# Performance work log

Measured on AMD Instinct MI355X. Metric: run time of the kernel, lower is better.

The kernel has to match this reference:

```python
import jax, jax.numpy as jnp
import numpy as np

N = 262144
H = 256
R = 32


def setup_inputs() -> dict:
    key = jax.random.key(0)
    ks = jax.random.split(key, 16)
    s = 1.0 / np.sqrt(H)
    return {
        "x": jax.random.normal(ks[0], (N, 1), jnp.float32),
        "t": jax.random.uniform(ks[1], (N, 1), jnp.float32),
        "start_w": jax.random.normal(ks[2], (H, 2), jnp.float32) * 0.5,
        "start_b": jax.random.normal(ks[3], (H,), jnp.float32) * 0.1,
        "end_w": jax.random.normal(ks[4], (1, H), jnp.float32) * s,
        "end_b": jax.random.normal(ks[5], (1,), jnp.float32) * 0.1,
        "col_0": jax.random.normal(ks[6], (H, R), jnp.float32) * s,
        "col_1": jax.random.normal(ks[7], (H, R), jnp.float32) * s,
        "col_2": jax.random.normal(ks[8], (H, R), jnp.float32) * s,
        "row_0": jax.random.normal(ks[9], (H, R), jnp.float32) * s,
        "row_1": jax.random.normal(ks[10], (H, R), jnp.float32) * s,
        "row_2": jax.random.normal(ks[11], (H, R), jnp.float32) * s,
        "alpha_0": jax.random.normal(ks[12], (R,), jnp.float32),
        "alpha_1": jax.random.normal(ks[13], (R,), jnp.float32),
        "alpha_2": jax.random.normal(ks[14], (R,), jnp.float32),
    }


def reference(x, t, start_w, start_b, end_w, end_b,
              col_0, col_1, col_2, row_0, row_1, row_2,
              alpha_0, alpha_1, alpha_2):
    # inputs: [N,2] -> start Linear -> tanh
    inp = jnp.concatenate([x, t], axis=1)
    h = jnp.tanh(inp @ start_w.T + start_b)  # [N, H]
    # three low-rank blocks: h @ (col * diag(alpha)) @ row.T, then tanh.
    # col_basis @ diag(alpha) == col_basis * alpha[None, :] (column scaling)
    for col, row, alpha in ((col_0, row_0, alpha_0),
                            (col_1, row_1, alpha_1),
                            (col_2, row_2, alpha_2)):
        h = jnp.tanh((h @ (col * alpha)) @ row.T)  # [N,H]->[N,R]->[N,H]
    return h @ end_w.T + end_b  # [N, 1]
```

## Files before the change

### kernel.cpp

```cpp
#include <hip/hip_runtime.h>


typedef _Float16 half4_t __attribute__((ext_vector_type(4)));
typedef __fp16   fp16x2  __attribute__((ext_vector_type(2)));
typedef float    float4_t __attribute__((ext_vector_type(4)));

#define TANH_SCALE 2.885390081777927f
#define MFMA16 __builtin_amdgcn_mfma_f32_16x16x16f16
#define NFRAG (3 * 16 * 2 * 64)

namespace {

struct alignas(16) Smem {
  half4_t ctf[NFRAG];
  float w0[256], w1[256], bb[256];
  float ew[256];
};

__device__ __forceinline__ half4_t pack4(float4_t v) {
  union { fp16x2 f2[2]; half4_t h4; } u;
  u.f2[0] = __builtin_amdgcn_cvt_pkrtz(v.x, v.y);
  u.f2[1] = __builtin_amdgcn_cvt_pkrtz(v.z, v.w);
  return u.h4;
}

__device__ __forceinline__ float tanh_pre(float y) {
  const float e = __builtin_amdgcn_exp2f(y);
  return fmaf(-2.0f, __builtin_amdgcn_rcpf(e + 1.0f), 1.0f);
}

__device__ __forceinline__ half4_t tanh4(float4_t v) {
  float4_t r;
  r.x = tanh_pre(v.x); r.y = tanh_pre(v.y);
  r.z = tanh_pre(v.z); r.w = tanh_pre(v.w);
  return pack4(r);
}

__global__ __launch_bounds__(1024) void stage_rwf(
    const float* __restrict__ r0, const float* __restrict__ r1,
    const float* __restrict__ r2, half4_t* __restrict__ ws)
{
  const int e = blockIdx.x * 1024 + threadIdx.x;
  if (e >= NFRAG) return;
  const int lane_ = e & 63;
  const int sel   = (e >> 6) & 1;
  const int t_    = (e >> 7) & 15;
  const int k_    = e >> 11;
  const int m_ = lane_ & 15, q_ = lane_ >> 4;
  const float* rk = (k_ == 0) ? r0 : (k_ == 1) ? r1 : r2;
  const int j = 16 * t_ + m_;
  const int rr = sel * 16 + 4 * q_;
  half4_t v;
  v.x = (_Float16)(rk[j * 32 + rr + 0] * TANH_SCALE);
  v.y = (_Float16)(rk[j * 32 + rr + 1] * TANH_SCALE);
  v.z = (_Float16)(rk[j * 32 + rr + 2] * TANH_SCALE);
  v.w = (_Float16)(rk[j * 32 + rr + 3] * TANH_SCALE);
  ws[e] = v;
}

__global__ __launch_bounds__(1024)
__attribute__((amdgpu_waves_per_eu(8, 8)))
void pinn_fused(
    const float* __restrict__ xg, const float* __restrict__ tg,
    const float* __restrict__ sw, const float* __restrict__ sb,
    const float* __restrict__ ewp, const float* __restrict__ ebp,
    const float* __restrict__ c0, const float* __restrict__ c1,
    const float* __restrict__ c2, const float* __restrict__ a0,
    const float* __restrict__ a1, const float* __restrict__ a2,
    const half4_t* __restrict__ rwg, float* __restrict__ out, int n)
{
  __shared__ Smem sm;
  const int tid = threadIdx.x;

  for (int e = tid; e < NFRAG; e += 1024) {
    const int lane_ = e & 63;
    const int sel   = (e >> 6) & 1;
    const int t_    = (e >> 7) & 15;
    const int k_    = e >> 11;
    const int m_ = lane_ & 15, q_ = lane_ >> 4;
    const float* ck = (k_ == 0) ? c0 : (k_ == 1) ? c1 : c2;
    const float* ak = (k_ == 0) ? a0 : (k_ == 1) ? a1 : a2;
    const int r = sel * 16 + m_;
    const float av = ak[r];
    const int j0 = 16 * t_ + 4 * q_;
    half4_t v;
    v.x = (_Float16)(ck[(j0 + 0) * 32 + r] * av);
    v.y = (_Float16)(ck[(j0 + 1) * 32 + r] * av);
    v.z = (_Float16)(ck[(j0 + 2) * 32 + r] * av);
    v.w = (_Float16)(ck[(j0 + 3) * 32 + r] * av);
    sm.ctf[e] = v;
  }
  if (tid < 256) {
    sm.w0[tid] = sw[2 * tid] * TANH_SCALE;
    sm.w1[tid] = sw[2 * tid + 1] * TANH_SCALE;
    sm.bb[tid] = sb[tid] * TANH_SCALE;
    sm.ew[tid] = ewp[tid];
  }
  __syncthreads();

  const int wave = tid >> 6;
  const int lane = tid & 63;
  const int m = lane & 15;
  const int q = lane >> 4;
  const int wo = 4 * q;
  const float ebv = ebp[0];
  const int tiles = n >> 4;

  const float4_t z4 = {0.f, 0.f, 0.f, 0.f};

#pragma unroll 1
  for (int g = (blockIdx.x * 16 + wave) * 2; g < tiles; g += 16384) {
    const int n0 = g * 16;
    const int n1 = n0 + 16;
    const float xm0 = xg[n0 + m], tm0 = tg[n0 + m];
    const float xm1 = xg[n1 + m], tm1 = tg[n1 + m];

    float4_t a00 = z4, a01 = z4, a10 = z4, a11 = z4;
    const half4_t* cp0 = &sm.ctf[lane];
#pragma unroll 1
    for (int t = 0; t < 16; ++t) {
      const int cb = t * 16 + wo;
      const float4_t w0v = *(const float4_t*)&sm.w0[cb];
      const float4_t w1v = *(const float4_t*)&sm.w1[cb];
      const float4_t bv  = *(const float4_t*)&sm.bb[cb];
      float4_t z0, z1;
      z0.x = fmaf(xm0, w0v.x, fmaf(tm0, w1v.x, bv.x));
      z1.x = fmaf(xm1, w0v.x, fmaf(tm1, w1v.x, bv.x));
      z0.y = fmaf(xm0, w0v.y, fmaf(tm0, w1v.y, bv.y));
      z1.y = fmaf(xm1, w0v.y, fmaf(tm1, w1v.y, bv.y));
      z0.z = fmaf(xm0, w0v.z, fmaf(tm0, w1v.z, bv.z));
      z1.z = fmaf(xm1, w0v.z, fmaf(tm1, w1v.z, bv.z));
      z0.w = fmaf(xm0, w0v.w, fmaf(tm0, w1v.w, bv.w));
      z1.w = fmaf(xm1, w0v.w, fmaf(tm1, w1v.w, bv.w));
      const half4_t h0 = tanh4(z0);
      const half4_t h1 = tanh4(z1);
      const half4_t cA = cp0[0], cB = cp0[64];
      a00 = MFMA16(cA, h0, a00, 0, 0, 0);
      a10 = MFMA16(cA, h1, a10, 0, 0, 0);
      a01 = MFMA16(cB, h0, a01, 0, 0, 0);
      a11 = MFMA16(cB, h1, a11, 0, 0, 0);
      cp0 += 128;
    }

#pragma unroll 1
    for (int k = 0; k < 2; ++k) {
      const half4_t pA0 = pack4(a00), pB0 = pack4(a01);
      const half4_t pA1 = pack4(a10), pB1 = pack4(a11);
      float4_t n00 = z4, n01 = z4, n10 = z4, n11 = z4;
      const half4_t* rp = &rwg[k * 2048 + lane];
      const half4_t* cp = &sm.ctf[(k + 1) * 2048 + lane];
#pragma unroll 1
      for (int t = 0; t < 16; ++t) {
        const half4_t rA = rp[0], rB = rp[64];
        const half4_t cA = cp[0], cB = cp[64];
        float4_t u0 = MFMA16(rA, pA0, z4, 0, 0, 0);
        float4_t u1 = MFMA16(rA, pA1, z4, 0, 0, 0);
        u0 = MFMA16(rB, pB0, u0, 0, 0, 0);
        u1 = MFMA16(rB, pB1, u1, 0, 0, 0);
        const half4_t h0 = tanh4(u0);
        const half4_t h1 = tanh4(u1);
        n00 = MFMA16(cA, h0, n00, 0, 0, 0);
        n10 = MFMA16(cA, h1, n10, 0, 0, 0);
        n01 = MFMA16(cB, h0, n01, 0, 0, 0);
        n11 = MFMA16(cB, h1, n11, 0, 0, 0);
        rp += 128; cp += 128;
      }
      a00 = n00; a01 = n01; a10 = n10; a11 = n11;
    }

    float ssum0 = 0.0f, ssum1 = 0.0f;
    {
      const half4_t pA0 = pack4(a00), pB0 = pack4(a01);
      const half4_t pA1 = pack4(a10), pB1 = pack4(a11);
      const half4_t* rp = &rwg[2 * 2048 + lane];
#pragma unroll 1
      for (int t = 0; t < 16; ++t) {
        const half4_t rA = rp[0], rB = rp[64];
        const float4_t ev = *(const float4_t*)&sm.ew[t * 16 + wo];
        float4_t u0 = MFMA16(rA, pA0, z4, 0, 0, 0);
        float4_t u1 = MFMA16(rA, pA1, z4, 0, 0, 0);
        u0 = MFMA16(rB, pB0, u0, 0, 0, 0);
        u1 = MFMA16(rB, pB1, u1, 0, 0, 0);
        ssum0 = fmaf(ev.x, tanh_pre(u0.x), ssum0);
        ssum1 = fmaf(ev.x, tanh_pre(u1.x), ssum1);
        ssum0 = fmaf(ev.y, tanh_pre(u0.y), ssum0);
        ssum1 = fmaf(ev.y, tanh_pre(u1.y), ssum1);
        ssum0 = fmaf(ev.z, tanh_pre(u0.z), ssum0);
        ssum1 = fmaf(ev.z, tanh_pre(u1.z), ssum1);
        ssum0 = fmaf(ev.w, tanh_pre(u0.w), ssum0);
        ssum1 = fmaf(ev.w, tanh_pre(u1.w), ssum1);
        rp += 128;
      }
    }

    ssum0 += __shfl_xor(ssum0, 16);
    ssum0 += __shfl_xor(ssum0, 32);
    ssum1 += __shfl_xor(ssum1, 16);
    ssum1 += __shfl_xor(ssum1, 32);
    if (lane < 16) {
      out[n0 + m] = ssum0 + ebv;
      out[n1 + m] = ssum1 + ebv;
    }
  }
}

}

extern "C" void kernel_launch(void* const* d_in, const int* in_sizes, int n_in,
                              void* d_out, int out_size, void* d_ws, size_t ws_size,
                              hipStream_t stream) {
  const float* xg  = (const float*)d_in[0];
  const float* tg  = (const float*)d_in[1];
  const float* sw  = (const float*)d_in[2];
  const float* sb  = (const float*)d_in[3];
  const float* ewp = (const float*)d_in[4];
  const float* ebp = (const float*)d_in[5];
  const float* c0  = (const float*)d_in[6];
  const float* c1  = (const float*)d_in[7];
  const float* c2  = (const float*)d_in[8];
  const float* r0  = (const float*)d_in[9];
  const float* r1  = (const float*)d_in[10];
  const float* r2  = (const float*)d_in[11];
  const float* a0  = (const float*)d_in[12];
  const float* a1  = (const float*)d_in[13];
  const float* a2  = (const float*)d_in[14];
  float* outp = (float*)d_out;
  half4_t* ws = (half4_t*)d_ws;

  const int n = in_sizes[0];

  stage_rwf<<<(NFRAG + 1023) / 1024, 1024, 0, stream>>>(r0, r1, r2, ws);

  pinn_fused<<<512, 1024, 0, stream>>>(xg, tg, sw, sb, ewp, ebp,
                                       c0, c1, c2, a0, a1, a2,
                                       ws, outp, n);
}
```

Baseline: 144.9 us.

## Fold tanh affine term into weights and bias, unroll middle loop by two

Rewrites tanh as 1 - 2*sigmoid-like term so each activation computes only rcp(exp2+1). The -2 scale is folded into the column weights and the end weights, and the constant part is handled by precomputed row sums used as accumulator init and output bias. This removes one FMA per activation. The middle-layer inner loop is also unrolled by two so more independent MFMAs are in flight. The risks are extra setup work per block, higher register pressure, and fp16 rounding of the folded -2 scaled weights plus rounding differences in the row sums.

Measured after the change: 153.2 us. +5.8%, slower.

```diff
diff --git a/kernel.cpp b/kernel.cpp
--- a/kernel.cpp
+++ b/kernel.cpp
@@ -15,6 +15,7 @@
   half4_t ctf[NFRAG];
   float w0[256], w1[256], bb[256];
   float ew[256];
+  float rsC[3 * 32];
 };
 
 __device__ __forceinline__ half4_t pack4(float4_t v) {
@@ -24,15 +25,14 @@
   return u.h4;
 }
 
-__device__ __forceinline__ float tanh_pre(float y) {
-  const float e = __builtin_amdgcn_exp2f(y);
-  return fmaf(-2.0f, __builtin_amdgcn_rcpf(e + 1.0f), 1.0f);
-}
-
-__device__ __forceinline__ half4_t tanh4(float4_t v) {
+__device__ __forceinline__ float inv_pre(float y) {
+  return __builtin_amdgcn_rcpf(__builtin_amdgcn_exp2f(y) + 1.0f);
+}
+
+__device__ __forceinline__ half4_t inv4(float4_t v) {
   float4_t r;
-  r.x = tanh_pre(v.x); r.y = tanh_pre(v.y);
-  r.z = tanh_pre(v.z); r.w = tanh_pre(v.w);
+  r.x = inv_pre(v.x); r.y = inv_pre(v.y);
+  r.z = inv_pre(v.z); r.w = inv_pre(v.w);
   return pack4(r);
 }
 
@@ -81,7 +81,7 @@
     const float* ck = (k_ == 0) ? c0 : (k_ == 1) ? c1 : c2;
     const float* ak = (k_ == 0) ? a0 : (k_ == 1) ? a1 : a2;
     const int r = sel * 16 + m_;
-    const float av = ak[r];
+    const float av = ak[r] * -2.0f;
     const int j0 = 16 * t_ + 4 * q_;
     half4_t v;
     v.x = (_Float16)(ck[(j0 + 0) * 32 + r] * av);
@@ -94,7 +94,20 @@
     sm.w0[tid] = sw[2 * tid] * TANH_SCALE;
     sm.w1[tid] = sw[2 * tid + 1] * TANH_SCALE;
     sm.bb[tid] = sb[tid] * TANH_SCALE;
-    sm.ew[tid] = ewp[tid];
+    sm.ew[tid] = ewp[tid] * -2.0f;
+  }
+  __syncthreads();
+
+  if (tid < 96) {
+    const int k_ = tid >> 5, r = tid & 31;
+    const int sel = r >> 4, mm = r & 15;
+    float s = 0.0f;
+    for (int t = 0; t < 16; ++t)
+      for (int qq = 0; qq < 4; ++qq) {
+        const half4_t v = sm.ctf[((k_ * 16 + t) * 2 + sel) * 64 + 16 * qq + mm];
+        s += (float)v.x + (float)v.y + (float)v.z + (float)v.w;
+      }
+    sm.rsC[k_ * 32 + r] = -0.5f * s;
   }
   __syncthreads();
 
@@ -106,6 +119,13 @@
   const float ebv = ebp[0];
   const int tiles = n >> 4;
 
+  float ewsum = 0.0f;
+  for (int t = 0; t < 16; ++t) {
+    const float4_t e4 = *(const float4_t*)&sm.ew[t * 16 + wo];
+    ewsum += e4.x + e4.y + e4.z + e4.w;
+  }
+  ewsum *= -0.5f;
+
   const float4_t z4 = {0.f, 0.f, 0.f, 0.f};
 
 #pragma unroll 1
@@ -115,7 +135,9 @@
     const float xm0 = xg[n0 + m], tm0 = tg[n0 + m];
     const float xm1 = xg[n1 + m], tm1 = tg[n1 + m];
 
-    float4_t a00 = z4, a01 = z4, a10 = z4, a11 = z4;
+    const float4_t rs00 = *(const float4_t*)&sm.rsC[wo];
+    const float4_t rs01 = *(const float4_t*)&sm.rsC[16 + wo];
+    float4_t a00 = rs00, a01 = rs01, a10 = rs00, a11 = rs01;
     const half4_t* cp0 = &sm.ctf[lane];
 #pragma unroll 1
     for (int t = 0; t < 16; ++t) {
@@ -132,8 +154,8 @@
       z1.z = fmaf(xm1, w0v.z, fmaf(tm1, w1v.z, bv.z));
       z0.w = fmaf(xm0, w0v.w, fmaf(tm0, w1v.w, bv.w));
       z1.w = fmaf(xm1, w0v.w, fmaf(tm1, w1v.w, bv.w));
-      const half4_t h0 = tanh4(z0);
-      const half4_t h1 = tanh4(z1);
+      const half4_t h0 = inv4(z0);
+      const half4_t h1 = inv4(z1);
       const half4_t cA = cp0[0], cB = cp0[64];
       a00 = MFMA16(cA, h0, a00, 0, 0, 0);
       a10 = MFMA16(cA, h1, a10, 0, 0, 0);
@@ -146,29 +168,43 @@
     for (int k = 0; k < 2; ++k) {
       const half4_t pA0 = pack4(a00), pB0 = pack4(a01);
       const half4_t pA1 = pack4(a10), pB1 = pack4(a11);
-      float4_t n00 = z4, n01 = z4, n10 = z4, n11 = z4;
+      const float4_t rsA = *(const float4_t*)&sm.rsC[(k + 1) * 32 + wo];
+      const float4_t rsB = *(const float4_t*)&sm.rsC[(k + 1) * 32 + 16 + wo];
+      float4_t n00 = rsA, n01 = rsB, n10 = rsA, n11 = rsB;
       const half4_t* rp = &rwg[k * 2048 + lane];
       const half4_t* cp = &sm.ctf[(k + 1) * 2048 + lane];
 #pragma unroll 1
-      for (int t = 0; t < 16; ++t) {
+      for (int t = 0; t < 8; ++t) {
         const half4_t rA = rp[0], rB = rp[64];
+        const half4_t rC = rp[128], rD = rp[192];
         const half4_t cA = cp[0], cB = cp[64];
+        const half4_t cC = cp[128], cD = cp[192];
         float4_t u0 = MFMA16(rA, pA0, z4, 0, 0, 0);
         float4_t u1 = MFMA16(rA, pA1, z4, 0, 0, 0);
+        float4_t v0 = MFMA16(rC, pA0, z4, 0, 0, 0);
+        float4_t v1 = MFMA16(rC, pA1, z4, 0, 0, 0);
         u0 = MFMA16(rB, pB0, u0, 0, 0, 0);
         u1 = MFMA16(rB, pB1, u1, 0, 0, 0);
-        const half4_t h0 = tanh4(u0);
-        const half4_t h1 = tanh4(u1);
+        v0 = MFMA16(rD, pB0, v0, 0, 0, 0);
+        v1 = MFMA16(rD, pB1, v1, 0, 0, 0);
+        const half4_t h0 = inv4(u0);
+        const half4_t h1 = inv4(u1);
+        const half4_t h2 = inv4(v0);
+        const half4_t h3 = inv4(v1);
         n00 = MFMA16(cA, h0, n00, 0, 0, 0);
         n10 = MFMA16(cA, h1, n10, 0, 0, 0);
         n01 = MFMA16(cB, h0, n01, 0, 0, 0);
         n11 = MFMA16(cB, h1, n11, 0, 0, 0);
-        rp += 128; cp += 128;
+        n00 = MFMA16(cC, h2, n00, 0, 0, 0);
+        n10 = MFMA16(cC, h3, n10, 0, 0, 0);
+        n01 = MFMA16(cD, h2, n01, 0, 0, 0);
+        n11 = MFMA16(cD, h3, n11, 0, 0, 0);
+        rp += 256; cp += 256;
       }
       a00 = n00; a01 = n01; a10 = n10; a11 = n11;
     }
 
-    float ssum0 = 0.0f, ssum1 = 0.0f;
+    float ssum0 = ewsum, ssum1 = ewsum;
     {
       const half4_t pA0 = pack4(a00), pB0 = pack4(a01);
       const half4_t pA1 = pack4(a10), pB1 = pack4(a11);
@@ -181,14 +217,14 @@
         float4_t u1 = MFMA16(rA, pA1, z4, 0, 0, 0);
         u0 = MFMA16(rB, pB0, u0, 0, 0, 0);
         u1 = MFMA16(rB, pB1, u1, 0, 0, 0);
-        ssum0 = fmaf(ev.x, tanh_pre(u0.x), ssum0);
-        ssum1 = fmaf(ev.x, tanh_pre(u1.x), ssum1);
-        ssum0 = fmaf(ev.y, tanh_pre(u0.y), ssum0);
-        ssum1 = fmaf(ev.y, tanh_pre(u1.y), ssum1);
-        ssum0 = fmaf(ev.z, tanh_pre(u0.z), ssum0);
-        ssum1 = fmaf(ev.z, tanh_pre(u1.z), ssum1);
-        ssum0 = fmaf(ev.w, tanh_pre(u0.w), ssum0);
-        ssum1 = fmaf(ev.w, tanh_pre(u1.w), ssum1);
+        ssum0 = fmaf(ev.x, inv_pre(u0.x), ssum0);
+        ssum1 = fmaf(ev.x, inv_pre(u1.x), ssum1);
+        ssum0 = fmaf(ev.y, inv_pre(u0.y), ssum0);
+        ssum1 = fmaf(ev.y, inv_pre(u1.y), ssum1);
+        ssum0 = fmaf(ev.z, inv_pre(u0.z), ssum0);
+        ssum1 = fmaf(ev.z, inv_pre(u1.z), ssum1);
+        ssum0 = fmaf(ev.w, inv_pre(u0.w), ssum0);
+        ssum1 = fmaf(ev.w, inv_pre(u1.w), ssum1);
         rp += 128;
       }
     }
```
